# Kernel optimization log

Hardware: AMD Instinct MI355X
Metric: run time of the kernel (lower is better)

## Reference

```python
import jax, jax.numpy as jnp
import numpy as np

HEADS = 8
DIM_HEAD = 64
SCALE = DIM_HEAD ** -0.5


def setup_inputs() -> dict:
    key = jax.random.key(0)
    ks = jax.random.split(key, 7)
    B, Nq, Nc = 4, 2048, 2048
    Dq, Dc = 1024, 768
    inner = HEADS * DIM_HEAD  # 512
    x = jax.random.normal(ks[0], (B, Nq, Dq), dtype=jnp.float32)
    context = jax.random.normal(ks[1], (B, Nc, Dc), dtype=jnp.float32)
    # Linear weights stored as (in, out) so y = x @ W, matching torch Linear math.
    Wq = jax.random.normal(ks[2], (Dq, inner), dtype=jnp.float32) * (Dq ** -0.5)
    Wk = jax.random.normal(ks[3], (Dc, inner), dtype=jnp.float32) * (Dc ** -0.5)
    Wv = jax.random.normal(ks[4], (Dc, inner), dtype=jnp.float32) * (Dc ** -0.5)
    Wo = jax.random.normal(ks[5], (inner, Dq), dtype=jnp.float32) * (inner ** -0.5)
    bo = jax.random.normal(ks[6], (Dq,), dtype=jnp.float32) * 0.01
    return {"x": x, "context": context, "Wq": Wq, "Wk": Wk, "Wv": Wv, "Wo": Wo, "bo": bo}


def reference(x, context, Wq, Wk, Wv, Wo, bo):
    B, Nq, _ = x.shape
    # projections -> [b, n, h, d]
    q = (x @ Wq).reshape(B, Nq, HEADS, DIM_HEAD)
    k = (context @ Wk).reshape(B, context.shape[1], HEADS, DIM_HEAD)
    v = (context @ Wv).reshape(B, context.shape[1], HEADS, DIM_HEAD)
    # scores [b, h, i, j]
    sim = jnp.einsum('bihd,bjhd->bhij', q, k) * SCALE
    attn = jax.nn.softmax(sim, axis=-1)
    out = jnp.einsum('bhij,bjhd->bihd', attn, v)  # [b, i, h, d]
    out = out.reshape(B, Nq, HEADS * DIM_HEAD)
    return out @ Wo + bo
```

## Files before the change

### kernel.cpp

```cpp
#include <hip/hip_runtime.h>
#include <hip/hip_bf16.h>


typedef __bf16 bf16_8 __attribute__((ext_vector_type(8)));
typedef __bf16 bf16_4 __attribute__((ext_vector_type(4)));
typedef float f32_4 __attribute__((ext_vector_type(4)));
typedef float f32_16 __attribute__((ext_vector_type(16)));
typedef int i32x2 __attribute__((ext_vector_type(2)));
typedef int i32x4 __attribute__((ext_vector_type(4)));

#define AS1 __attribute__((address_space(1)))
#define AS3 __attribute__((address_space(3)))

__device__ __forceinline__ void gld_lds16(const __bf16* g, __bf16* l) {
  __builtin_amdgcn_global_load_lds((AS1 unsigned int*)(void*)g,
                                   (AS3 unsigned int*)(void*)l, 16, 0, 0);
}

__device__ __forceinline__ int cvt_pk(float lo, float hi) {
  int r;
  __asm__("v_cvt_pk_bf16_f32 %0, %1, %2" : "=v"(r) : "v"(lo), "v"(hi));
  return r;
}

__global__ __launch_bounds__(256) void prep(
    const float* __restrict__ x, const float* __restrict__ ctx,
    const float* __restrict__ Wq, const float* __restrict__ Wk,
    const float* __restrict__ Wv, const float* __restrict__ Wo,
    __bf16* __restrict__ xb, __bf16* __restrict__ ctxb,
    __bf16* __restrict__ WqT, __bf16* __restrict__ WkT,
    __bf16* __restrict__ WvT, __bf16* __restrict__ WoT) {
  int tb = blockIdx.x;
  if (tb >= 1792) {
    tb -= 1792;
    const float* src;
    __bf16* dst;
    size_t base;
    if (tb < 4096) { src = x; dst = xb; base = (size_t)tb * 2048; }
    else { src = ctx; dst = ctxb; base = (size_t)(tb - 4096) * 2048; }
    const size_t idx = base + threadIdx.x * 8;
    const f32_4 f0 = *(const f32_4*)(src + idx);
    const f32_4 f1 = *(const f32_4*)(src + idx + 4);
    bf16_8 v;
#pragma unroll
    for (int i = 0; i < 4; ++i) { v[i] = (__bf16)f0[i]; v[4 + i] = (__bf16)f1[i]; }
    *(bf16_8*)(dst + idx) = v;
    return;
  }
  __shared__ __bf16 t[32][33];
  const float* W; __bf16* Wt; int K, N;
  if (tb < 512)       { W = Wq; Wt = WqT; K = 1024; N = 512; }
  else if (tb < 896)  { tb -= 512;  W = Wk; Wt = WkT; K = 768; N = 512; }
  else if (tb < 1280) { tb -= 896;  W = Wv; Wt = WvT; K = 768; N = 512; }
  else                { tb -= 1280; W = Wo; Wt = WoT; K = 512; N = 1024; }
  const int nx = N >> 5;
  const int n0 = (tb % nx) * 32, k0 = (tb / nx) * 32;
  const int tx = threadIdx.x & 31, ty = threadIdx.x >> 5;
#pragma unroll
  for (int r = 0; r < 32; r += 8)
    t[ty + r][tx] = (__bf16)W[(size_t)(k0 + ty + r) * N + n0 + tx];
  __syncthreads();
#pragma unroll
  for (int r = 0; r < 32; r += 8)
    Wt[(size_t)(n0 + ty + r) * K + k0 + tx] = t[tx][ty + r];
}

__global__ __launch_bounds__(256, 2) void proj(
    const __bf16* __restrict__ xb, const __bf16* __restrict__ ctxb,
    const __bf16* __restrict__ WqT, const __bf16* __restrict__ WkvT,
    __bf16* __restrict__ Qb, __bf16* __restrict__ Kbuf,
    __bf16* __restrict__ Vtb) {
  __shared__ __align__(16) __bf16 As[2][128 * 64];
  __shared__ __align__(16) __bf16 Bs[2][128 * 64];
  int tb = blockIdx.x;
  const __bf16 *A, *Bt;
  int K, bm, bn, mode;
  if (tb < 256) {
    A = xb; Bt = WqT; K = 1024; mode = 0;
    bn = (tb & 3) << 7; bm = (tb >> 2) << 7;
  } else {
    tb -= 256;
    A = ctxb; Bt = WkvT; K = 768; mode = 1;
    bn = (tb & 7) << 7; bm = (tb >> 3) << 7;
  }
  const int tid = threadIdx.x;
  const int lane = tid & 63;
  const int wave = tid >> 6;
  const int wi = (wave >> 1) * 64;
  const int wn = (wave & 1) * 64;
  const int lrow = lane & 15;
  const int quad = lane >> 4;
  const int lkey = lrow & 7;
  const int srow = tid >> 3;
  const int scol = (tid & 7) * 8;
  const int swz = (((scol >> 3) ^ (srow & 7)) * 8);

  f32_4 acc[4][4];
#pragma unroll
  for (int i = 0; i < 4; ++i)
#pragma unroll
    for (int j = 0; j < 4; ++j)
#pragma unroll
      for (int r = 0; r < 4; ++r) acc[i][j][r] = 0.0f;

  auto stage = [&](int buf, int kt) {
#pragma unroll
    for (int r = 0; r < 4; ++r) {
      const int row = r * 32 + srow;
      gld_lds16(A + (size_t)(bm + row) * K + kt + swz, &As[buf][row * 64 + scol]);
    }
#pragma unroll
    for (int r = 0; r < 4; ++r) {
      const int row = r * 32 + srow;
      gld_lds16(Bt + (size_t)(bn + row) * K + kt + swz, &Bs[buf][row * 64 + scol]);
    }
  };

  stage(0, 0);
  const int nkt = K >> 6;
  for (int kti = 0; kti < nkt; ++kti) {
    __syncthreads();
    if (kti + 1 < nkt) stage((kti + 1) & 1, (kti + 1) * 64);
    const __bf16* Asb = As[kti & 1];
    const __bf16* Bsb = Bs[kti & 1];
#pragma unroll
    for (int ks = 0; ks < 2; ++ks) {
      bf16_8 af[4], bfv[4];
#pragma unroll
      for (int t = 0; t < 4; ++t)
        af[t] = *(const bf16_8*)(Asb + (wi + t * 16 + lrow) * 64 +
                                 (((ks * 4 + quad) ^ lkey) * 8));
#pragma unroll
      for (int t = 0; t < 4; ++t)
        bfv[t] = *(const bf16_8*)(Bsb + (wn + t * 16 + lrow) * 64 +
                                  (((ks * 4 + quad) ^ lkey) * 8));
#pragma unroll
      for (int it = 0; it < 4; ++it)
#pragma unroll
        for (int nt = 0; nt < 4; ++nt)
          acc[it][nt] = __builtin_amdgcn_mfma_f32_16x16x32_bf16(
              af[it], bfv[nt], acc[it][nt], 0, 0, 0);
    }
  }

#pragma unroll
  for (int nt = 0; nt < 4; ++nt) {
    const int c = bn + wn + nt * 16 + lrow;
    if (mode == 0) {
#pragma unroll
      for (int it = 0; it < 4; ++it) {
        const int rbase = bm + wi + it * 16 + quad * 4;
#pragma unroll
        for (int r = 0; r < 4; ++r)
          Qb[(size_t)(rbase + r) * 512 + c] = (__bf16)(acc[it][nt][r] * 0.125f);
      }
    } else if (c < 512) {
#pragma unroll
      for (int it = 0; it < 4; ++it) {
        const int rbase = bm + wi + it * 16 + quad * 4;
#pragma unroll
        for (int r = 0; r < 4; ++r)
          Kbuf[(size_t)(rbase + r) * 512 + c] = (__bf16)acc[it][nt][r];
      }
    } else {
      const int vcol = c - 512;
      const int bhh = ((bm >> 11) << 3) + (vcol >> 6);
      const int d = vcol & 63;
#pragma unroll
      for (int it = 0; it < 4; ++it) {
        const int jb = (bm & 2047) + wi + it * 16 + quad * 4;
        bf16_4 pk;
#pragma unroll
        for (int r = 0; r < 4; ++r) pk[r] = (__bf16)acc[it][nt][r];
        *(bf16_4*)&Vtb[((size_t)(bhh * 64 + d)) * 2048 + jb] = pk;
      }
    }
  }
}

__global__ __launch_bounds__(512, 4) void attn_fwd(const __bf16* __restrict__ Q,
                                                   const __bf16* __restrict__ Kb,
                                                   const __bf16* __restrict__ Vt,
                                                   __bf16* __restrict__ AO) {
  __shared__ __align__(16) __bf16 KVs[4][2][64 * 64];
  __shared__ __align__(16) float Ls[8][32];
  const int tid = threadIdx.x;
  const int lane = tid & 63;
  const int wave = tid >> 6;
  const int wq = wave & 3;
  const int jhalf = wave >> 2;
  const int did = blockIdx.x;
  const int sid = did >> 3;
  const int bh = ((did & 7) << 2) + (sid & 3);
  const int ib = sid >> 2;
  const int b = bh >> 3, h = bh & 7;
  const int i0 = ib * 128 + wq * 32;
  const int li = lane & 31;
  const int hi = lane >> 5;
  const int key = li & 7;
  const size_t bq = (size_t)b * 2048;
  const int hc = h * 64;

  const int ssub = lane >> 3;
  const int sch = lane & 7;
  const int sswz = (sch ^ ssub) * 8;

  const __bf16* Kg = Kb + bq * 512 + hc;
  const __bf16* Vg = Vt + (size_t)bh * 64 * 2048;
  __bf16* Ksl = &KVs[jhalf * 2 + 0][0][0];
  __bf16* Vsl = &KVs[jhalf * 2 + 1][0][0];

  auto stage = [&](int buf, int j0) {
#pragma unroll
    for (int t = 0; t < 2; ++t) {
      const int rb = wq * 16 + t * 8;
      gld_lds16(Kg + (size_t)(j0 + rb + ssub) * 512 + sswz,
                Ksl + buf * 4096 + rb * 64);
      gld_lds16(Vg + (size_t)(rb + ssub) * 2048 + j0 + sswz,
                Vsl + buf * 4096 + rb * 64);
    }
  };

  bf16_8 aq[4];
#pragma unroll
  for (int ks = 0; ks < 4; ++ks)
    aq[ks] = *(const bf16_8*)(Q + (bq + i0 + li) * 512 + hc + ks * 16 + hi * 8);

  float psl = 0.0f;
  f32_16 oacc[2];
#pragma unroll
  for (int d = 0; d < 2; ++d)
#pragma unroll
    for (int r = 0; r < 16; ++r) oacc[d][r] = 0.0f;

  auto softmax_h = [&](const f32_16& s, int pwo[2][4]) {
    float p[16];
#pragma unroll
    for (int r = 0; r < 16; ++r) p[r] = __expf(s[r]);
    float e0 = 0.0f, e1 = 0.0f;
#pragma unroll
    for (int r = 0; r < 8; ++r) { e0 += p[2 * r]; e1 += p[2 * r + 1]; }
    psl += e0 + e1;
    const int c01 = cvt_pk(p[0], p[1]),   c23 = cvt_pk(p[2], p[3]);
    const int c45 = cvt_pk(p[4], p[5]),   c67 = cvt_pk(p[6], p[7]);
    const int c89 = cvt_pk(p[8], p[9]),   cab = cvt_pk(p[10], p[11]);
    const int ccd = cvt_pk(p[12], p[13]), cef = cvt_pk(p[14], p[15]);
    const i32x2 r02 = __builtin_amdgcn_permlane32_swap(c01, c45, false, false);
    const i32x2 r13 = __builtin_amdgcn_permlane32_swap(c23, c67, false, false);
    const i32x2 r46 = __builtin_amdgcn_permlane32_swap(c89, ccd, false, false);
    const i32x2 r57 = __builtin_amdgcn_permlane32_swap(cab, cef, false, false);
    pwo[0][0] = r02[0]; pwo[0][1] = r13[0]; pwo[0][2] = r02[1]; pwo[0][3] = r13[1];
    pwo[1][0] = r46[0]; pwo[1][1] = r57[0]; pwo[1][2] = r46[1]; pwo[1][3] = r57[1];
  };

  const int jbase = jhalf * 1024;
  stage(0, jbase);

  for (int jt = 0; jt < 16; ++jt) {
    __syncthreads();
    if (jt + 1 < 16) stage((jt + 1) & 1, jbase + (jt + 1) * 64);
    const __bf16* Ksb = Ksl + (jt & 1) * 4096;
    const __bf16* Vsb = Vsl + (jt & 1) * 4096;

    auto pvq = [&](const int pwk[4], int ks2) {
      i32x4 w4;
      w4[0] = pwk[0]; w4[1] = pwk[1]; w4[2] = pwk[2]; w4[3] = pwk[3];
      const bf16_8 ap = __builtin_bit_cast(bf16_8, w4);
#pragma unroll
      for (int dblk = 0; dblk < 2; ++dblk) {
        const bf16_8 bv = *(const bf16_8*)(
            Vsb + (dblk * 32 + li) * 64 + (((ks2 * 2 + hi) ^ key) * 8));
        oacc[dblk] = __builtin_amdgcn_mfma_f32_32x32x16_bf16(
            ap, bv, oacc[dblk], 0, 0, 0);
      }
    };

    __builtin_amdgcn_s_setprio(1);
    f32_16 s0, s1;
#pragma unroll
    for (int r = 0; r < 16; ++r) { s0[r] = 0.0f; s1[r] = 0.0f; }
#pragma unroll
    for (int ks = 0; ks < 4; ++ks) {
      const bf16_8 ak = *(const bf16_8*)(
          Ksb + li * 64 + (((ks * 2 + hi) ^ key) * 8));
      s0 = __builtin_amdgcn_mfma_f32_32x32x16_bf16(ak, aq[ks], s0, 0, 0, 0);
    }
#pragma unroll
    for (int ks = 0; ks < 4; ++ks) {
      const bf16_8 ak = *(const bf16_8*)(
          Ksb + (32 + li) * 64 + (((ks * 2 + hi) ^ key) * 8));
      s1 = __builtin_amdgcn_mfma_f32_32x32x16_bf16(ak, aq[ks], s1, 0, 0, 0);
    }
    int pwA[2][4], pwB[2][4];
    softmax_h(s0, pwA);
    pvq(pwA[0], 0);
    pvq(pwA[1], 1);
    softmax_h(s1, pwB);
    pvq(pwB[0], 2);
    pvq(pwB[1], 3);
    __builtin_amdgcn_s_setprio(0);
  }

  __syncthreads();
  float* Cs = (float*)&KVs[0][0][0];

  const float tot = psl + __shfl_xor(psl, 32);
  if (lane < 32) Ls[wave][li] = tot;

  if (jhalf == 1) {
    float* Cw = Cs + wq * 2048;
#pragma unroll
    for (int dblk = 0; dblk < 2; ++dblk)
#pragma unroll
      for (int g = 0; g < 4; ++g)
#pragma unroll
        for (int r = 0; r < 4; ++r)
          Cw[(8 * g + 4 * hi + r) * 64 + dblk * 32 + li] = oacc[dblk][4 * g + r];
  }
  __syncthreads();

  if (jhalf == 0) {
    const float* Cw = Cs + wq * 2048;
    f32_4 s0v[4], s1v[4];
#pragma unroll
    for (int g = 0; g < 4; ++g) {
      s0v[g] = *(const f32_4*)(&Ls[wq][8 * g + 4 * hi]);
      s1v[g] = *(const f32_4*)(&Ls[wq + 4][8 * g + 4 * hi]);
    }
#pragma unroll
    for (int dblk = 0; dblk < 2; ++dblk)
#pragma unroll
      for (int g = 0; g < 4; ++g)
#pragma unroll
        for (int r = 0; r < 4; ++r) {
          const int rl = 8 * g + 4 * hi + r;
          const float o = oacc[dblk][4 * g + r] + Cw[rl * 64 + dblk * 32 + li];
          const float inv = 1.0f / (s0v[g][r] + s1v[g][r]);
          const size_t rg = bq + i0 + rl;
          AO[rg * 512 + hc + dblk * 32 + li] = (__bf16)(o * inv);
        }
  }
}

__global__ __launch_bounds__(256, 2) void gemm_out(const __bf16* __restrict__ A,
                                                   const __bf16* __restrict__ Bt,
                                                   float* __restrict__ C,
                                                   const float* __restrict__ bias) {
  __shared__ __align__(16) __bf16 As[2][128 * 64];
  __shared__ __align__(16) __bf16 Bs[2][128 * 64];
  const int K = 512, N = 1024;
  const int tid = threadIdx.x;
  const int lane = tid & 63;
  const int wave = tid >> 6;
  const int wi = (wave >> 1) * 64;
  const int wn = (wave & 1) * 64;
  const int bm = blockIdx.y * 128;
  const int bn = blockIdx.x * 128;
  const int lrow = lane & 15;
  const int quad = lane >> 4;
  const int lkey = lrow & 7;
  const int srow = tid >> 3;
  const int scol = (tid & 7) * 8;
  const int swz = (((scol >> 3) ^ (srow & 7)) * 8);

  f32_4 acc[4][4];
#pragma unroll
  for (int i = 0; i < 4; ++i)
#pragma unroll
    for (int j = 0; j < 4; ++j)
#pragma unroll
      for (int r = 0; r < 4; ++r) acc[i][j][r] = 0.0f;

  auto stage = [&](int buf, int kt) {
#pragma unroll
    for (int r = 0; r < 4; ++r) {
      const int row = r * 32 + srow;
      gld_lds16(A + (size_t)(bm + row) * K + kt + swz, &As[buf][row * 64 + scol]);
      gld_lds16(Bt + (size_t)(bn + row) * K + kt + swz, &Bs[buf][row * 64 + scol]);
    }
  };

  stage(0, 0);
  for (int kti = 0; kti < 8; ++kti) {
    __syncthreads();
    if (kti + 1 < 8) stage((kti + 1) & 1, (kti + 1) * 64);
    const __bf16* Asb = As[kti & 1];
    const __bf16* Bsb = Bs[kti & 1];
#pragma unroll
    for (int ks = 0; ks < 2; ++ks) {
      bf16_8 af[4], bfv[4];
#pragma unroll
      for (int t = 0; t < 4; ++t)
        af[t] = *(const bf16_8*)(Asb + (wi + t * 16 + lrow) * 64 +
                                 (((ks * 4 + quad) ^ lkey) * 8));
#pragma unroll
      for (int t = 0; t < 4; ++t)
        bfv[t] = *(const bf16_8*)(Bsb + (wn + t * 16 + lrow) * 64 +
                                  (((ks * 4 + quad) ^ lkey) * 8));
#pragma unroll
      for (int it = 0; it < 4; ++it)
#pragma unroll
        for (int nt = 0; nt < 4; ++nt)
          acc[it][nt] = __builtin_amdgcn_mfma_f32_16x16x32_bf16(
              af[it], bfv[nt], acc[it][nt], 0, 0, 0);
    }
  }

#pragma unroll
  for (int nt = 0; nt < 4; ++nt) {
    const int c = bn + wn + nt * 16 + lrow;
    const float bv = bias[c];
#pragma unroll
    for (int it = 0; it < 4; ++it) {
      const int rbase = bm + wi + it * 16 + quad * 4;
#pragma unroll
      for (int r = 0; r < 4; ++r)
        C[(size_t)(rbase + r) * N + c] = acc[it][nt][r] + bv;
    }
  }
}

extern "C" void kernel_launch(void* const* d_in, const int* in_sizes, int n_in,
                              void* d_out, int out_size, void* d_ws, size_t ws_size,
                              hipStream_t stream) {
  (void)in_sizes; (void)n_in; (void)out_size; (void)ws_size;
  const float* x   = (const float*)d_in[0];
  const float* ctx = (const float*)d_in[1];
  const float* Wq  = (const float*)d_in[2];
  const float* Wk  = (const float*)d_in[3];
  const float* Wv  = (const float*)d_in[4];
  const float* Wo  = (const float*)d_in[5];
  const float* bo  = (const float*)d_in[6];

  __bf16* ws = (__bf16*)d_ws;
  __bf16* WqT  = ws;
  __bf16* WkT  = WqT + 512 * 1024;
  __bf16* WvT  = WkT + 512 * 768;
  __bf16* WoT  = WvT + 512 * 768;
  __bf16* Qb   = WoT + 1024 * 512;
  __bf16* Kbuf = Qb + 8192 * 512;
  __bf16* Vtb  = Kbuf + 8192 * 512;
  __bf16* AOb  = Vtb + 8192 * 512;
  __bf16* xb   = AOb + 8192 * 512;
  __bf16* ctxb = xb + 8192 * 1024;

  prep<<<8960, 256, 0, stream>>>(x, ctx, Wq, Wk, Wv, Wo,
                                 xb, ctxb, WqT, WkT, WvT, WoT);

  proj<<<768, 256, 0, stream>>>(xb, ctxb, WqT, WkT, Qb, Kbuf, Vtb);

  attn_fwd<<<512, 512, 0, stream>>>(Qb, Kbuf, Vtb, AOb);

  gemm_out<<<dim3(8, 64), 256, 0, stream>>>(AOb, WoT, (float*)d_out, bo);
}
```

Measured before the change: 210.2 us.

## Process 64 query rows per wave in attention to reuse K/V fragments

Each attention wave now handles two 32-row query tiles instead of one. The K and V fragments are loaded from LDS once per tile and feed MFMAs for both query tiles, with the QK, softmax and PV stages interleaved across them. The grid is halved to 256 blocks and launch bounds are lowered to match. This cuts LDS read traffic per unit of compute but raises register pressure and leaves fewer resident blocks to hide latency. The epilogue's cross-half reduction buffer now fills the whole 64 KB K/V staging area.

```diff
diff --git a/kernel.cpp b/kernel.cpp
--- a/kernel.cpp
+++ b/kernel.cpp
@@ -178,12 +178,12 @@
   }
 }
 
-__global__ __launch_bounds__(512, 4) void attn_fwd(const __bf16* __restrict__ Q,
+__global__ __launch_bounds__(512, 2) void attn_fwd(const __bf16* __restrict__ Q,
                                                    const __bf16* __restrict__ Kb,
                                                    const __bf16* __restrict__ Vt,
                                                    __bf16* __restrict__ AO) {
   __shared__ __align__(16) __bf16 KVs[4][2][64 * 64];
-  __shared__ __align__(16) float Ls[8][32];
+  __shared__ __align__(16) float Ls[8][64];
   const int tid = threadIdx.x;
   const int lane = tid & 63;
   const int wave = tid >> 6;
@@ -194,7 +194,7 @@
   const int bh = ((did & 7) << 2) + (sid & 3);
   const int ib = sid >> 2;
   const int b = bh >> 3, h = bh & 7;
-  const int i0 = ib * 128 + wq * 32;
+  const int i0 = ib * 256 + wq * 64;
   const int li = lane & 31;
   const int hi = lane >> 5;
   const int key = li & 7;
@@ -221,26 +221,28 @@
     }
   };
 
-  bf16_8 aq[4];
-#pragma unroll
-  for (int ks = 0; ks < 4; ++ks)
-    aq[ks] = *(const bf16_8*)(Q + (bq + i0 + li) * 512 + hc + ks * 16 + hi * 8);
-
-  float psl = 0.0f;
-  f32_16 oacc[2];
+  bf16_8 aq0[4], aq1[4];
+#pragma unroll
+  for (int ks = 0; ks < 4; ++ks) {
+    aq0[ks] = *(const bf16_8*)(Q + (bq + i0 + li) * 512 + hc + ks * 16 + hi * 8);
+    aq1[ks] = *(const bf16_8*)(Q + (bq + i0 + 32 + li) * 512 + hc + ks * 16 + hi * 8);
+  }
+
+  float psl0 = 0.0f, psl1 = 0.0f;
+  f32_16 oacc0[2], oacc1[2];
 #pragma unroll
   for (int d = 0; d < 2; ++d)
 #pragma unroll
-    for (int r = 0; r < 16; ++r) oacc[d][r] = 0.0f;
-
-  auto softmax_h = [&](const f32_16& s, int pwo[2][4]) {
+    for (int r = 0; r < 16; ++r) { oacc0[d][r] = 0.0f; oacc1[d][r] = 0.0f; }
+
+  auto softmax_h = [&](const f32_16& s, int pwo[2][4], float& psum) {
     float p[16];
 #pragma unroll
     for (int r = 0; r < 16; ++r) p[r] = __expf(s[r]);
     float e0 = 0.0f, e1 = 0.0f;
 #pragma unroll
     for (int r = 0; r < 8; ++r) { e0 += p[2 * r]; e1 += p[2 * r + 1]; }
-    psl += e0 + e1;
+    psum += e0 + e1;
     const int c01 = cvt_pk(p[0], p[1]),   c23 = cvt_pk(p[2], p[3]);
     const int c45 = cvt_pk(p[4], p[5]),   c67 = cvt_pk(p[6], p[7]);
     const int c89 = cvt_pk(p[8], p[9]),   cab = cvt_pk(p[10], p[11]);
@@ -262,83 +264,108 @@
     const __bf16* Ksb = Ksl + (jt & 1) * 4096;
     const __bf16* Vsb = Vsl + (jt & 1) * 4096;
 
-    auto pvq = [&](const int pwk[4], int ks2) {
-      i32x4 w4;
-      w4[0] = pwk[0]; w4[1] = pwk[1]; w4[2] = pwk[2]; w4[3] = pwk[3];
-      const bf16_8 ap = __builtin_bit_cast(bf16_8, w4);
+    __builtin_amdgcn_s_setprio(1);
+    bf16_8 ak[2][4];
+#pragma unroll
+    for (int jb = 0; jb < 2; ++jb)
+#pragma unroll
+      for (int ks = 0; ks < 4; ++ks)
+        ak[jb][ks] = *(const bf16_8*)(
+            Ksb + (jb * 32 + li) * 64 + (((ks * 2 + hi) ^ key) * 8));
+
+    f32_16 s0, s1;
+#pragma unroll
+    for (int r = 0; r < 16; ++r) { s0[r] = 0.0f; s1[r] = 0.0f; }
+#pragma unroll
+    for (int ks = 0; ks < 4; ++ks) {
+      s0 = __builtin_amdgcn_mfma_f32_32x32x16_bf16(ak[0][ks], aq0[ks], s0, 0, 0, 0);
+      s1 = __builtin_amdgcn_mfma_f32_32x32x16_bf16(ak[1][ks], aq0[ks], s1, 0, 0, 0);
+    }
+    int pw0A[2][4], pw0B[2][4];
+    softmax_h(s0, pw0A, psl0);
+    f32_16 t0, t1;
+#pragma unroll
+    for (int r = 0; r < 16; ++r) { t0[r] = 0.0f; t1[r] = 0.0f; }
+#pragma unroll
+    for (int ks = 0; ks < 4; ++ks) {
+      t0 = __builtin_amdgcn_mfma_f32_32x32x16_bf16(ak[0][ks], aq1[ks], t0, 0, 0, 0);
+      t1 = __builtin_amdgcn_mfma_f32_32x32x16_bf16(ak[1][ks], aq1[ks], t1, 0, 0, 0);
+    }
+    softmax_h(s1, pw0B, psl0);
+    int pw1A[2][4], pw1B[2][4];
+    softmax_h(t0, pw1A, psl1);
+    softmax_h(t1, pw1B, psl1);
+
+    bf16_8 bv[2][4];
+#pragma unroll
+    for (int dblk = 0; dblk < 2; ++dblk)
+#pragma unroll
+      for (int ks2 = 0; ks2 < 4; ++ks2)
+        bv[dblk][ks2] = *(const bf16_8*)(
+            Vsb + (dblk * 32 + li) * 64 + (((ks2 * 2 + hi) ^ key) * 8));
+
+    auto pv_step = [&](const int w0[4], const int w1[4], int ks2) {
+      i32x4 a0, a1;
+      a0[0] = w0[0]; a0[1] = w0[1]; a0[2] = w0[2]; a0[3] = w0[3];
+      a1[0] = w1[0]; a1[1] = w1[1]; a1[2] = w1[2]; a1[3] = w1[3];
+      const bf16_8 ap0 = __builtin_bit_cast(bf16_8, a0);
+      const bf16_8 ap1 = __builtin_bit_cast(bf16_8, a1);
 #pragma unroll
       for (int dblk = 0; dblk < 2; ++dblk) {
-        const bf16_8 bv = *(const bf16_8*)(
-            Vsb + (dblk * 32 + li) * 64 + (((ks2 * 2 + hi) ^ key) * 8));
-        oacc[dblk] = __builtin_amdgcn_mfma_f32_32x32x16_bf16(
-            ap, bv, oacc[dblk], 0, 0, 0);
+        oacc0[dblk] = __builtin_amdgcn_mfma_f32_32x32x16_bf16(
+            ap0, bv[dblk][ks2], oacc0[dblk], 0, 0, 0);
+        oacc1[dblk] = __builtin_amdgcn_mfma_f32_32x32x16_bf16(
+            ap1, bv[dblk][ks2], oacc1[dblk], 0, 0, 0);
       }
     };
-
-    __builtin_amdgcn_s_setprio(1);
-    f32_16 s0, s1;
-#pragma unroll
-    for (int r = 0; r < 16; ++r) { s0[r] = 0.0f; s1[r] = 0.0f; }
-#pragma unroll
-    for (int ks = 0; ks < 4; ++ks) {
-      const bf16_8 ak = *(const bf16_8*)(
-          Ksb + li * 64 + (((ks * 2 + hi) ^ key) * 8));
-      s0 = __builtin_amdgcn_mfma_f32_32x32x16_bf16(ak, aq[ks], s0, 0, 0, 0);
-    }
-#pragma unroll
-    for (int ks = 0; ks < 4; ++ks) {
-      const bf16_8 ak = *(const bf16_8*)(
-          Ksb + (32 + li) * 64 + (((ks * 2 + hi) ^ key) * 8));
-      s1 = __builtin_amdgcn_mfma_f32_32x32x16_bf16(ak, aq[ks], s1, 0, 0, 0);
-    }
-    int pwA[2][4], pwB[2][4];
-    softmax_h(s0, pwA);
-    pvq(pwA[0], 0);
-    pvq(pwA[1], 1);
-    softmax_h(s1, pwB);
-    pvq(pwB[0], 2);
-    pvq(pwB[1], 3);
+    pv_step(pw0A[0], pw1A[0], 0);
+    pv_step(pw0A[1], pw1A[1], 1);
+    pv_step(pw0B[0], pw1B[0], 2);
+    pv_step(pw0B[1], pw1B[1], 3);
     __builtin_amdgcn_s_setprio(0);
   }
 
   __syncthreads();
   float* Cs = (float*)&KVs[0][0][0];
 
-  const float tot = psl + __shfl_xor(psl, 32);
-  if (lane < 32) Ls[wave][li] = tot;
+  const float tot0 = psl0 + __shfl_xor(psl0, 32);
+  const float tot1 = psl1 + __shfl_xor(psl1, 32);
+  if (lane < 32) { Ls[wave][li] = tot0; Ls[wave][32 + li] = tot1; }
 
   if (jhalf == 1) {
-    float* Cw = Cs + wq * 2048;
+    float* Cw = Cs + wq * 4096;
 #pragma unroll
     for (int dblk = 0; dblk < 2; ++dblk)
 #pragma unroll
       for (int g = 0; g < 4; ++g)
 #pragma unroll
-        for (int r = 0; r < 4; ++r)
-          Cw[(8 * g + 4 * hi + r) * 64 + dblk * 32 + li] = oacc[dblk][4 * g + r];
+        for (int r = 0; r < 4; ++r) {
+          Cw[(8 * g + 4 * hi + r) * 64 + dblk * 32 + li] = oacc0[dblk][4 * g + r];
+          Cw[(32 + 8 * g + 4 * hi + r) * 64 + dblk * 32 + li] = oacc1[dblk][4 * g + r];
+        }
   }
   __syncthreads();
 
   if (jhalf == 0) {
-    const float* Cw = Cs + wq * 2048;
-    f32_4 s0v[4], s1v[4];
-#pragma unroll
-    for (int g = 0; g < 4; ++g) {
-      s0v[g] = *(const f32_4*)(&Ls[wq][8 * g + 4 * hi]);
-      s1v[g] = *(const f32_4*)(&Ls[wq + 4][8 * g + 4 * hi]);
-    }
-#pragma unroll
-    for (int dblk = 0; dblk < 2; ++dblk)
-#pragma unroll
-      for (int g = 0; g < 4; ++g)
-#pragma unroll
-        for (int r = 0; r < 4; ++r) {
-          const int rl = 8 * g + 4 * hi + r;
-          const float o = oacc[dblk][4 * g + r] + Cw[rl * 64 + dblk * 32 + li];
-          const float inv = 1.0f / (s0v[g][r] + s1v[g][r]);
-          const size_t rg = bq + i0 + rl;
-          AO[rg * 512 + hc + dblk * 32 + li] = (__bf16)(o * inv);
-        }
+    const float* Cw = Cs + wq * 4096;
+#pragma unroll
+    for (int it = 0; it < 2; ++it)
+#pragma unroll
+      for (int g = 0; g < 4; ++g) {
+        const int rb = it * 32 + 8 * g + 4 * hi;
+        const f32_4 sa = *(const f32_4*)(&Ls[wq][rb]);
+        const f32_4 sb = *(const f32_4*)(&Ls[wq + 4][rb]);
+#pragma unroll
+        for (int dblk = 0; dblk < 2; ++dblk)
+#pragma unroll
+          for (int r = 0; r < 4; ++r) {
+            const int rl = rb + r;
+            const float mine = it ? oacc1[dblk][4 * g + r] : oacc0[dblk][4 * g + r];
+            const float o = mine + Cw[rl * 64 + dblk * 32 + li];
+            const float inv = 1.0f / (sa[r] + sb[r]);
+            AO[(bq + i0 + rl) * 512 + hc + dblk * 32 + li] = (__bf16)(o * inv);
+          }
+      }
   }
 }
 
@@ -449,7 +476,7 @@
 
   proj<<<768, 256, 0, stream>>>(xb, ctxb, WqT, WkT, Qb, Kbuf, Vtb);
 
-  attn_fwd<<<512, 512, 0, stream>>>(Qb, Kbuf, Vtb, AOb);
+  attn_fwd<<<256, 512, 0, stream>>>(Qb, Kbuf, Vtb, AOb);
 
   gemm_out<<<dim3(8, 64), 256, 0, stream>>>(AOb, WoT, (float*)d_out, bo);
 }
```

Measured after the change: 211.7 us. About the same (+0.7%).

## Load V fragments directly from global, use exp2 with log2e-folded Q scale

Applied to the files above, without the earlier changes.

The attention kernel no longer stages V tiles through LDS. Each wave now loads its V fragments straight from global memory into registers at the start of each key tile, which halves LDS use and the async copy traffic. Softmax switches from __expf to the hardware exp2, with log2(e) folded into the Q projection scale, and the first QK MFMA starts from a zero accumulator instead of zeroing in a loop. The launch bound drops from 4 to 2 to make room for the extra registers. The trade-off is less coalesced global loads for V and higher register pressure, which may lower occupancy.

```diff
diff --git a/kernel.cpp b/kernel.cpp
--- a/kernel.cpp
+++ b/kernel.cpp
@@ -152,7 +152,8 @@
         const int rbase = bm + wi + it * 16 + quad * 4;
 #pragma unroll
         for (int r = 0; r < 4; ++r)
-          Qb[(size_t)(rbase + r) * 512 + c] = (__bf16)(acc[it][nt][r] * 0.125f);
+          Qb[(size_t)(rbase + r) * 512 + c] =
+              (__bf16)(acc[it][nt][r] * 0.18033688011112042f);
       }
     } else if (c < 512) {
 #pragma unroll
@@ -178,11 +179,11 @@
   }
 }
 
-__global__ __launch_bounds__(512, 4) void attn_fwd(const __bf16* __restrict__ Q,
+__global__ __launch_bounds__(512, 2) void attn_fwd(const __bf16* __restrict__ Q,
                                                    const __bf16* __restrict__ Kb,
                                                    const __bf16* __restrict__ Vt,
                                                    __bf16* __restrict__ AO) {
-  __shared__ __align__(16) __bf16 KVs[4][2][64 * 64];
+  __shared__ __align__(16) __bf16 Ks[2][2][64 * 64];
   __shared__ __align__(16) float Ls[8][32];
   const int tid = threadIdx.x;
   const int lane = tid & 63;
@@ -207,8 +208,7 @@
 
   const __bf16* Kg = Kb + bq * 512 + hc;
   const __bf16* Vg = Vt + (size_t)bh * 64 * 2048;
-  __bf16* Ksl = &KVs[jhalf * 2 + 0][0][0];
-  __bf16* Vsl = &KVs[jhalf * 2 + 1][0][0];
+  __bf16* Ksl = &Ks[jhalf][0][0];
 
   auto stage = [&](int buf, int j0) {
 #pragma unroll
@@ -216,8 +216,6 @@
       const int rb = wq * 16 + t * 8;
       gld_lds16(Kg + (size_t)(j0 + rb + ssub) * 512 + sswz,
                 Ksl + buf * 4096 + rb * 64);
-      gld_lds16(Vg + (size_t)(rb + ssub) * 2048 + j0 + sswz,
-                Vsl + buf * 4096 + rb * 64);
     }
   };
 
@@ -226,6 +224,10 @@
   for (int ks = 0; ks < 4; ++ks)
     aq[ks] = *(const bf16_8*)(Q + (bq + i0 + li) * 512 + hc + ks * 16 + hi * 8);
 
+  f32_16 z16;
+#pragma unroll
+  for (int r = 0; r < 16; ++r) z16[r] = 0.0f;
+
   float psl = 0.0f;
   f32_16 oacc[2];
 #pragma unroll
@@ -236,7 +238,7 @@
   auto softmax_h = [&](const f32_16& s, int pwo[2][4]) {
     float p[16];
 #pragma unroll
-    for (int r = 0; r < 16; ++r) p[r] = __expf(s[r]);
+    for (int r = 0; r < 16; ++r) p[r] = __builtin_amdgcn_exp2f(s[r]);
     float e0 = 0.0f, e1 = 0.0f;
 #pragma unroll
     for (int r = 0; r < 8; ++r) { e0 += p[2 * r]; e1 += p[2 * r + 1]; }
@@ -258,35 +260,45 @@
 
   for (int jt = 0; jt < 16; ++jt) {
     __syncthreads();
+
+    bf16_8 bv[2][4];
+#pragma unroll
+    for (int dblk = 0; dblk < 2; ++dblk)
+#pragma unroll
+      for (int ks2 = 0; ks2 < 4; ++ks2)
+        bv[dblk][ks2] = *(const bf16_8*)(
+            Vg + (size_t)(dblk * 32 + li) * 2048 + jbase + jt * 64 +
+            ks2 * 16 + hi * 8);
+
     if (jt + 1 < 16) stage((jt + 1) & 1, jbase + (jt + 1) * 64);
     const __bf16* Ksb = Ksl + (jt & 1) * 4096;
-    const __bf16* Vsb = Vsl + (jt & 1) * 4096;
 
     auto pvq = [&](const int pwk[4], int ks2) {
       i32x4 w4;
       w4[0] = pwk[0]; w4[1] = pwk[1]; w4[2] = pwk[2]; w4[3] = pwk[3];
       const bf16_8 ap = __builtin_bit_cast(bf16_8, w4);
 #pragma unroll
-      for (int dblk = 0; dblk < 2; ++dblk) {
-        const bf16_8 bv = *(const bf16_8*)(
-            Vsb + (dblk * 32 + li) * 64 + (((ks2 * 2 + hi) ^ key) * 8));
+      for (int dblk = 0; dblk < 2; ++dblk)
         oacc[dblk] = __builtin_amdgcn_mfma_f32_32x32x16_bf16(
-            ap, bv, oacc[dblk], 0, 0, 0);
-      }
+            ap, bv[dblk][ks2], oacc[dblk], 0, 0, 0);
     };
 
     __builtin_amdgcn_s_setprio(1);
     f32_16 s0, s1;
-#pragma unroll
-    for (int r = 0; r < 16; ++r) { s0[r] = 0.0f; s1[r] = 0.0f; }
-#pragma unroll
-    for (int ks = 0; ks < 4; ++ks) {
+    {
+      const bf16_8 ak0 = *(const bf16_8*)(Ksb + li * 64 + ((hi ^ key) * 8));
+      s0 = __builtin_amdgcn_mfma_f32_32x32x16_bf16(ak0, aq[0], z16, 0, 0, 0);
+      const bf16_8 bk0 = *(const bf16_8*)(Ksb + (32 + li) * 64 + ((hi ^ key) * 8));
+      s1 = __builtin_amdgcn_mfma_f32_32x32x16_bf16(bk0, aq[0], z16, 0, 0, 0);
+    }
+#pragma unroll
+    for (int ks = 1; ks < 4; ++ks) {
       const bf16_8 ak = *(const bf16_8*)(
           Ksb + li * 64 + (((ks * 2 + hi) ^ key) * 8));
       s0 = __builtin_amdgcn_mfma_f32_32x32x16_bf16(ak, aq[ks], s0, 0, 0, 0);
     }
 #pragma unroll
-    for (int ks = 0; ks < 4; ++ks) {
+    for (int ks = 1; ks < 4; ++ks) {
       const bf16_8 ak = *(const bf16_8*)(
           Ksb + (32 + li) * 64 + (((ks * 2 + hi) ^ key) * 8));
       s1 = __builtin_amdgcn_mfma_f32_32x32x16_bf16(ak, aq[ks], s1, 0, 0, 0);
@@ -302,7 +314,7 @@
   }
 
   __syncthreads();
-  float* Cs = (float*)&KVs[0][0][0];
+  float* Cs = (float*)&Ks[0][0][0];
 
   const float tot = psl + __shfl_xor(psl, 32);
   if (lane < 32) Ls[wave][li] = tot;
```

Result: slower. 258.3 us (+22.9%).
